# Kernel optimization log

Hardware: AMD Instinct MI355X
Metric: run time of the kernel (lower is better)

Reference implementation:

```python
import jax, jax.numpy as jnp
import numpy as np

B, N, C, H = 8, 4096, 768, 32
D = C // H  # head_dim = 24
EPS = 1e-12


def _l2norm(t):
    # F.normalize(dim=-1): t / max(||t||_2, eps)
    n = jnp.sqrt(jnp.sum(t * t, axis=-1, keepdims=True))
    return t / jnp.maximum(n, EPS)


def setup_inputs() -> dict:
    key = jax.random.key(0)
    ks = jax.random.split(key, 6)
    s_in = 1.0 / np.sqrt(C)
    return {
        "x": jax.random.normal(ks[0], (B, N, C), dtype=jnp.float32),
        "W_qkv": jax.random.uniform(ks[1], (C, 3 * C), jnp.float32, -s_in, s_in),
        "b_qkv": jax.random.uniform(ks[2], (3 * C,), jnp.float32, -s_in, s_in),
        "temperature": jnp.ones((H, 1, 1), dtype=jnp.float32),
        "W_proj": jax.random.uniform(ks[3], (C, C), jnp.float32, -s_in, s_in),
        "b_proj": jax.random.uniform(ks[4], (C,), jnp.float32, -s_in, s_in),
    }


def reference(x, W_qkv, b_qkv, temperature, W_proj, b_proj):
    b, n, c = x.shape
    qkv = x @ W_qkv + b_qkv                                  # (B,N,3C)
    qkv = qkv.reshape(b, n, 3, H, D).transpose(2, 0, 3, 1, 4)  # (3,B,H,N,D)
    q, k, v = qkv[0], qkv[1], qkv[2]                         # (B,H,N,D)
    q = jnp.swapaxes(q, -1, -2)                              # (B,H,D,N)
    k = jnp.swapaxes(k, -1, -2)
    v = jnp.swapaxes(v, -1, -2)
    q = _l2norm(q)                                           # normalize over N
    k = _l2norm(k)
    attn = jnp.einsum('bhdn,bhen->bhde', q, k) * temperature  # (B,H,D,D)
    attn = jax.nn.softmax(attn, axis=-1)
    y = jnp.einsum('bhde,bhen->bhdn', attn, v)               # (B,H,D,N)
    # Faithful to torch: (1,B,H,D,N).transpose(1,2).reshape(B,N,C)
    # == (H,B,D,N) flattened row-major into (B,N,C)
    y = jnp.transpose(y, (1, 0, 2, 3)).reshape(b, n, c)
    return y @ W_proj + b_proj
```

## Files before the change

kernel.cpp:

```cpp
#include <hip/hip_runtime.h>
#include <hip/hip_bf16.h>


#define DEVI __device__ __forceinline__

typedef __attribute__((ext_vector_type(8))) short bf16x8;
typedef __attribute__((ext_vector_type(4))) float f32x4;
typedef unsigned int u32;
typedef unsigned short u16;

DEVI u16 f2bf(float f) {
  union { float f; u32 u; } x; x.f = f;
  u32 r = x.u + 0x7FFFu + ((x.u >> 16) & 1u);
  return (u16)(r >> 16);
}

DEVI void gload_lds16(const void* g, void* l) {
  __builtin_amdgcn_global_load_lds((__attribute__((address_space(1))) void*)g,
                                   (__attribute__((address_space(3))) void*)l, 16, 0, 0);
}

__global__ __launch_bounds__(256) void cvt_kernel(const float* __restrict__ in,
                                                  u16* __restrict__ out, int n8) {
  int i = blockIdx.x * 256 + threadIdx.x;
  if (i >= n8) return;
  long o = (long)i * 8;
  float4 a = *(const float4*)(in + o);
  float4 b = *(const float4*)(in + o + 4);
  uint4 v;
  v.x = f2bf(a.x) | ((u32)f2bf(a.y) << 16);
  v.y = f2bf(a.z) | ((u32)f2bf(a.w) << 16);
  v.z = f2bf(b.x) | ((u32)f2bf(b.y) << 16);
  v.w = f2bf(b.z) | ((u32)f2bf(b.w) << 16);
  *(uint4*)(out + o) = v;
}

__global__ __launch_bounds__(256) void transpose_cvt(const float* __restrict__ W,
                                                     u16* __restrict__ Wt, int K, int N) {
  __shared__ float tile[32][33];
  int n0 = blockIdx.x * 32, k0 = blockIdx.y * 32;
  int tx = threadIdx.x, ty = threadIdx.y;
  #pragma unroll
  for (int i = 0; i < 4; ++i)
    tile[ty + 8 * i][tx] = W[(long)(k0 + ty + 8 * i) * N + n0 + tx];
  __syncthreads();
  #pragma unroll
  for (int i = 0; i < 4; ++i)
    Wt[(long)(n0 + ty + 8 * i) * K + k0 + tx] = f2bf(tile[tx][ty + 8 * i]);
}

template<int NT, int BF16_OUT>
__global__ __launch_bounds__(512, 4) void gemm2b_kernel(
    const u16* __restrict__ A, const u16* __restrict__ Bt,
    const float* __restrict__ bias, void* __restrict__ Cout,
    int M, int N) {
  constexpr int K = NT * 32;
  __shared__ __attribute__((aligned(128))) char lds[49152];

  int nbx = N >> 8;
  int nwg = gridDim.x;
  int bid = blockIdx.x;
  bid = (bid & 7) * (nwg >> 3) + (bid >> 3);
  int bx = bid % nbx, by = bid / nbx;

  int t = threadIdx.x;
  int w = t >> 6, l = t & 63;
  int wr = w >> 2, wc = w & 3;
  int l16 = l & 15, l4 = l >> 4;

  int cbb = (l4 * 16) ^ ((l16 & 8) << 2);
  int pA0 = (wr * 64 + l16) * 64 + cbb;
  int pB0 = 16384 + (wc * 64 + l16) * 64 + cbb;

  int pa = t * 16;
  int la = pa ^ (((pa >> 9) & 1) << 5);
  int soffA = (la >> 6) * K + ((la & 63) >> 1);
  int soffB[2];
  #pragma unroll
  for (int j = 0; j < 2; ++j) {
    int p = (j * 512 + t) * 16;
    int lb = p ^ (((p >> 9) & 1) << 5);
    soffB[j] = (lb >> 6) * K + ((lb & 63) >> 1);
  }

  const u16* Ag = A + (long)by * 128 * K;
  const u16* Bg = Bt + (long)bx * 256 * K;
  int sdst = w * 1024;

  f32x4 acc[4][4] = {};

  gload_lds16(Ag + soffA, lds + sdst);
  #pragma unroll
  for (int j = 0; j < 2; ++j)
    gload_lds16(Bg + soffB[j], lds + 16384 + j * 8192 + sdst);

  for (int kt = 0; kt < NT; ++kt) {
    int s = kt & 1;
    if (kt + 1 < NT) {
      gload_lds16(Ag + soffA + (kt + 1) * 32, lds + (s ^ 1) * 8192 + sdst);
      #pragma unroll
      for (int j = 0; j < 2; ++j)
        gload_lds16(Bg + soffB[j] + (kt + 1) * 32,
                    lds + 16384 + (s ^ 1) * 16384 + j * 8192 + sdst);
      asm volatile("s_waitcnt vmcnt(3)" ::: "memory");
    } else {
      asm volatile("s_waitcnt vmcnt(0)" ::: "memory");
    }
    __builtin_amdgcn_sched_barrier(0);
    __builtin_amdgcn_s_barrier();
    __builtin_amdgcn_sched_barrier(0);

    bf16x8 aF[4], bF[4];
    #pragma unroll
    for (int mi = 0; mi < 4; ++mi)
      aF[mi] = *(const bf16x8*)(lds + s * 8192 + mi * 1024 + pA0);
    #pragma unroll
    for (int n = 0; n < 4; ++n)
      bF[n] = *(const bf16x8*)(lds + s * 16384 + n * 1024 + pB0);

    __builtin_amdgcn_s_setprio(1);
    #pragma unroll
    for (int mi = 0; mi < 4; ++mi)
      #pragma unroll
      for (int n = 0; n < 4; ++n)
        acc[mi][n] = __builtin_amdgcn_mfma_f32_16x16x32_bf16(aF[mi], bF[n], acc[mi][n], 0, 0, 0);
    __builtin_amdgcn_s_setprio(0);
    __builtin_amdgcn_s_barrier();
    __builtin_amdgcn_sched_barrier(0);
  }

  #pragma unroll
  for (int mi = 0; mi < 4; ++mi) {
    int row0 = by * 128 + wr * 64 + mi * 16 + l4 * 4;
    #pragma unroll
    for (int n = 0; n < 4; ++n) {
      int col = bx * 256 + wc * 64 + n * 16 + l16;
      float bv = bias[col];
      #pragma unroll
      for (int j = 0; j < 4; ++j) {
        long idx = (long)(row0 + j) * N + col;
        float v = acc[mi][n][j] + bv;
        if (BF16_OUT) __builtin_nontemporal_store(f2bf(v), (u16*)Cout + idx);
        else          __builtin_nontemporal_store(v, (float*)Cout + idx);
      }
    }
  }
}

#define PFQK(nc, rq, rk)                                                       \
  { long cb = (long)(nc) * 294912;                                             \
    _Pragma("unroll") for (int i = 0; i < 6; ++i) {                            \
      rq[i] = *(const u32*)(qbase + cb + offi[i]);                             \
      rk[i] = *(const u32*)(qbase + cb + offi[i] + 768); } }

#define WRQK(rq, rk)                                                           \
  { _Pragma("unroll") for (int i = 0; i < 6; ++i) {                            \
      qt[dv[i] * 2][nv[i]] = (u16)rq[i];                                       \
      qt[dv[i] * 2 + 1][nv[i]] = (u16)(rq[i] >> 16);                           \
      kt[dv[i] * 2][nv[i]] = (u16)rk[i];                                       \
      kt[dv[i] * 2 + 1][nv[i]] = (u16)(rk[i] >> 16); } }

#define GRAM_MFMA                                                              \
  { _Pragma("unroll") for (int ks = 0; ks < 4; ++ks) {                         \
      int koff = ks * 32 + l4 * 8;                                             \
      bf16x8 qa = *(const bf16x8*)&qt[fm * 16 + l16][koff];                    \
      bf16x8 qb = *(const bf16x8*)&qt[fn * 16 + l16][koff];                    \
      bf16x8 ka = *(const bf16x8*)&kt[fm * 16 + l16][koff];                    \
      bf16x8 kb = *(const bf16x8*)&kt[fn * 16 + l16][koff];                    \
      accG = __builtin_amdgcn_mfma_f32_16x16x32_bf16(qa, kb, accG, 0, 0, 0);   \
      accQ = __builtin_amdgcn_mfma_f32_16x16x32_bf16(qa, qb, accQ, 0, 0, 0);   \
      accK = __builtin_amdgcn_mfma_f32_16x16x32_bf16(ka, kb, accK, 0, 0, 0); } }

#define PFV(nc, rv)                                                            \
  { long cb = (long)(nc) * 294912;                                             \
    _Pragma("unroll") for (int i = 0; i < 6; ++i)                              \
      rv[i] = *(const u32*)(vbase + cb + offi[i]); }

#define WRV(rv)                                                                \
  { _Pragma("unroll") for (int i = 0; i < 6; ++i)                              \
      *(u32*)&vl[nv[i]][dv[i] * 2] = rv[i]; }

#define PV_STORE(nc)                                                           \
  { int n0 = (nc) * 128;                                                       \
    f32x4 z = {};                                                              \
    _Pragma("unroll") for (int fnn = 0; fnn < 2; ++fnn) {                      \
      int ncol = w * 32 + fnn * 16 + l16;                                      \
      bf16x8 bv = *(const bf16x8*)&vl[ncol][l4 * 8];                           \
      f32x4 y0 = __builtin_amdgcn_mfma_f32_16x16x32_bf16(af0, bv, z, 0, 0, 0); \
      f32x4 y1 = __builtin_amdgcn_mfma_f32_16x16x32_bf16(af1, bv, z, 0, 0, 0); \
      int gn = n0 + ncol;                                                      \
      _Pragma("unroll") for (int j = 0; j < 4; ++j) {                          \
        int d0 = l4 * 4 + j;                                                   \
        ybase[(long)d0 * 4096 + gn] = f2bf(y0[j]);                             \
        int d1 = 16 + d0;                                                      \
        if (d1 < 24) ybase[(long)d1 * 4096 + gn] = f2bf(y1[j]); } } }

__global__ __launch_bounds__(256) void attn_kernel(const u16* __restrict__ qkv,
                                                   const float* __restrict__ temperature,
                                                   u16* __restrict__ yout) {
  __shared__ u16 qt[32][136];
  __shared__ u16 kt[32][136];
  __shared__ u16 vl[128][40];
  __shared__ u16 attnb[32][40];
  __shared__ float Gs[32][33];
  __shared__ float sq[32];
  __shared__ float sk[32];

  int bid = blockIdx.x;
  int b = bid >> 5, h = bid & 31;
  int t = threadIdx.x;
  int w = t >> 6, l = t & 63;
  int l16 = l & 15, l4 = l >> 4;
  int fm = w >> 1, fn = w & 1;

  for (int i = t; i < 32 * 136; i += 256) { qt[0][i] = 0; kt[0][i] = 0; }
  for (int i = t; i < 128 * 40; i += 256) vl[0][i] = 0;
  for (int i = t; i < 32 * 40; i += 256) attnb[0][i] = 0;

  int nv[6], dv[6], offi[6];
  #pragma unroll
  for (int i = 0; i < 6; ++i) {
    int idx = t + 256 * i;
    nv[i] = idx / 12; dv[i] = idx % 12;
    offi[i] = nv[i] * 2304 + dv[i] * 2;
  }

  f32x4 accG = {}, accQ = {}, accK = {};
  const u16* qbase = qkv + (long)b * 4096 * 2304 + h * 24;
  const u16* vbase = qbase + 1536;

  u32 rqA[6], rkA[6], rqB[6], rkB[6];
  PFQK(0, rqA, rkA);
  PFQK(1, rqB, rkB);
  __syncthreads();

  for (int nc = 0; nc < 32; nc += 2) {
    WRQK(rqA, rkA);
    __syncthreads();
    if (nc + 2 < 32) PFQK(nc + 2, rqA, rkA);
    GRAM_MFMA;
    __syncthreads();
    WRQK(rqB, rkB);
    __syncthreads();
    if (nc + 3 < 32) PFQK(nc + 3, rqB, rkB);
    GRAM_MFMA;
    __syncthreads();
  }

  #pragma unroll
  for (int j = 0; j < 4; ++j) Gs[fm * 16 + l4 * 4 + j][fn * 16 + l16] = accG[j];
  if (fm == fn) {
    #pragma unroll
    for (int j = 0; j < 4; ++j)
      if (l4 * 4 + j == l16) { sq[fm * 16 + l16] = accQ[j]; sk[fm * 16 + l16] = accK[j]; }
  }
  __syncthreads();

  if (t < 24) {
    float nq = fmaxf(sqrtf(fmaxf(sq[t], 0.f)), 1e-12f);
    float tmp = temperature[h];
    float p[24]; float mx = -1e30f;
    #pragma unroll
    for (int e = 0; e < 24; ++e) {
      float nk = fmaxf(sqrtf(fmaxf(sk[e], 0.f)), 1e-12f);
      float a = Gs[t][e] / (nq * nk) * tmp;
      p[e] = a; mx = fmaxf(mx, a);
    }
    float s = 0.f;
    #pragma unroll
    for (int e = 0; e < 24; ++e) { p[e] = __expf(p[e] - mx); s += p[e]; }
    float inv = 1.f / s;
    #pragma unroll
    for (int e = 0; e < 24; ++e) attnb[t][e] = f2bf(p[e] * inv);
  }

  u32 rvA[6], rvB[6];
  PFV(0, rvA);
  PFV(1, rvB);
  __syncthreads();

  bf16x8 af0 = *(const bf16x8*)&attnb[l16][l4 * 8];
  bf16x8 af1 = *(const bf16x8*)&attnb[16 + l16][l4 * 8];
  u16* ybase = yout + (long)(h * 8 + b) * 24 * 4096;

  for (int nc = 0; nc < 32; nc += 2) {
    WRV(rvA);
    __syncthreads();
    if (nc + 2 < 32) PFV(nc + 2, rvA);
    PV_STORE(nc);
    __syncthreads();
    WRV(rvB);
    __syncthreads();
    if (nc + 3 < 32) PFV(nc + 3, rvB);
    PV_STORE(nc + 1);
    __syncthreads();
  }
}

extern "C" void kernel_launch(void* const* d_in, const int* in_sizes, int n_in,
                              void* d_out, int out_size, void* d_ws, size_t ws_size,
                              hipStream_t stream) {
  const float* x     = (const float*)d_in[0];
  const float* Wqkv  = (const float*)d_in[1];
  const float* bqkv  = (const float*)d_in[2];
  const float* temp  = (const float*)d_in[3];
  const float* Wproj = (const float*)d_in[4];
  const float* bproj = (const float*)d_in[5];
  float* out = (float*)d_out;

  char* ws = (char*)d_ws;
  u16* xb  = (u16*)(ws);
  u16* wqt = (u16*)(ws + 50331648);
  u16* wpt = (u16*)(ws + 53870592);
  u16* qkv = (u16*)(ws + 55050240);
  u16* y   = xb;

  cvt_kernel<<<12288, 256, 0, stream>>>(x, xb, 3145728);
  transpose_cvt<<<dim3(72, 24), dim3(32, 8), 0, stream>>>(Wqkv, wqt, 768, 2304);
  transpose_cvt<<<dim3(24, 24), dim3(32, 8), 0, stream>>>(Wproj, wpt, 768, 768);
  gemm2b_kernel<24, 1><<<2304, 512, 0, stream>>>(xb, wqt, bqkv, qkv, 32768, 2304);
  attn_kernel<<<256, 256, 0, stream>>>(qkv, temp, y);
  gemm2b_kernel<24, 0><<<768, 512, 0, stream>>>(y, wpt, bproj, out, 32768, 768);
}
```

Baseline: 320.1 us.

## Triple-buffer GEMM K pipeline, widen attention chunk loads to 16-byte vectors

The bf16 GEMM moves from double to triple buffering in LDS, with two K tiles in flight and the loop fully unrolled, to hide more global load latency. The cost is more LDS per block (72KB), which may reduce occupancy. The attention kernel now processes 256-token chunks with uint4 (16-byte) loads instead of 4-byte loads, halving loop iterations and barriers, at the price of larger LDS tiles. The bf16 GEMM output store also changes from nontemporal to a regular store, so the qkv result can stay in cache for the attention kernel that reads it next.

```diff
diff --git a/kernel.cpp b/kernel.cpp
--- a/kernel.cpp
+++ b/kernel.cpp
@@ -49,13 +49,19 @@
     Wt[(long)(n0 + ty + 8 * i) * K + k0 + tx] = f2bf(tile[tx][ty + 8 * i]);
 }
 
+#define STAGE_T(ktile, slot)                                                   \
+  { gload_lds16(Ag + soffA + (ktile) * 32, lds + (slot) * 8192 + sdst);        \
+    _Pragma("unroll") for (int j_ = 0; j_ < 2; ++j_)                           \
+      gload_lds16(Bg + soffB[j_] + (ktile) * 32,                               \
+                  lds + 24576 + (slot) * 16384 + j_ * 8192 + sdst); }
+
 template<int NT, int BF16_OUT>
 __global__ __launch_bounds__(512, 4) void gemm2b_kernel(
     const u16* __restrict__ A, const u16* __restrict__ Bt,
     const float* __restrict__ bias, void* __restrict__ Cout,
     int M, int N) {
   constexpr int K = NT * 32;
-  __shared__ __attribute__((aligned(128))) char lds[49152];
+  __shared__ __attribute__((aligned(128))) char lds[73728];
 
   int nbx = N >> 8;
   int nwg = gridDim.x;
@@ -70,7 +76,7 @@
 
   int cbb = (l4 * 16) ^ ((l16 & 8) << 2);
   int pA0 = (wr * 64 + l16) * 64 + cbb;
-  int pB0 = 16384 + (wc * 64 + l16) * 64 + cbb;
+  int pB0 = (wc * 64 + l16) * 64 + cbb;
 
   int pa = t * 16;
   int la = pa ^ (((pa >> 9) & 1) << 5);
@@ -89,19 +95,16 @@
 
   f32x4 acc[4][4] = {};
 
-  gload_lds16(Ag + soffA, lds + sdst);
-  #pragma unroll
-  for (int j = 0; j < 2; ++j)
-    gload_lds16(Bg + soffB[j], lds + 16384 + j * 8192 + sdst);
-
+  STAGE_T(0, 0);
+  STAGE_T(1, 1);
+
+  #pragma unroll
   for (int kt = 0; kt < NT; ++kt) {
-    int s = kt & 1;
-    if (kt + 1 < NT) {
-      gload_lds16(Ag + soffA + (kt + 1) * 32, lds + (s ^ 1) * 8192 + sdst);
-      #pragma unroll
-      for (int j = 0; j < 2; ++j)
-        gload_lds16(Bg + soffB[j] + (kt + 1) * 32,
-                    lds + 16384 + (s ^ 1) * 16384 + j * 8192 + sdst);
+    int rs = kt % 3;
+    if (kt + 2 < NT) {
+      STAGE_T(kt + 2, (kt + 2) % 3);
+      asm volatile("s_waitcnt vmcnt(6)" ::: "memory");
+    } else if (kt + 2 == NT) {
       asm volatile("s_waitcnt vmcnt(3)" ::: "memory");
     } else {
       asm volatile("s_waitcnt vmcnt(0)" ::: "memory");
@@ -113,10 +116,10 @@
     bf16x8 aF[4], bF[4];
     #pragma unroll
     for (int mi = 0; mi < 4; ++mi)
-      aF[mi] = *(const bf16x8*)(lds + s * 8192 + mi * 1024 + pA0);
+      aF[mi] = *(const bf16x8*)(lds + rs * 8192 + mi * 1024 + pA0);
     #pragma unroll
     for (int n = 0; n < 4; ++n)
-      bF[n] = *(const bf16x8*)(lds + s * 16384 + n * 1024 + pB0);
+      bF[n] = *(const bf16x8*)(lds + 24576 + rs * 16384 + n * 1024 + pB0);
 
     __builtin_amdgcn_s_setprio(1);
     #pragma unroll
@@ -140,7 +143,7 @@
       for (int j = 0; j < 4; ++j) {
         long idx = (long)(row0 + j) * N + col;
         float v = acc[mi][n][j] + bv;
-        if (BF16_OUT) __builtin_nontemporal_store(f2bf(v), (u16*)Cout + idx);
+        if (BF16_OUT) ((u16*)Cout)[idx] = f2bf(v);
         else          __builtin_nontemporal_store(v, (float*)Cout + idx);
       }
     }
@@ -148,20 +151,22 @@
 }
 
 #define PFQK(nc, rq, rk)                                                       \
-  { long cb = (long)(nc) * 294912;                                             \
-    _Pragma("unroll") for (int i = 0; i < 6; ++i) {                            \
-      rq[i] = *(const u32*)(qbase + cb + offi[i]);                             \
-      rk[i] = *(const u32*)(qbase + cb + offi[i] + 768); } }
+  { long cb = (long)(nc) * 589824;                                             \
+    _Pragma("unroll") for (int i = 0; i < 3; ++i) {                            \
+      rq[i] = *(const uint4*)(qbase + cb + offI[i]);                           \
+      rk[i] = *(const uint4*)(kbase + cb + offI[i]); } }
 
 #define WRQK(rq, rk)                                                           \
-  { _Pragma("unroll") for (int i = 0; i < 6; ++i) {                            \
-      qt[dv[i] * 2][nv[i]] = (u16)rq[i];                                       \
-      qt[dv[i] * 2 + 1][nv[i]] = (u16)(rq[i] >> 16);                           \
-      kt[dv[i] * 2][nv[i]] = (u16)rk[i];                                       \
-      kt[dv[i] * 2 + 1][nv[i]] = (u16)(rk[i] >> 16); } }
-
-#define GRAM_MFMA                                                              \
-  { _Pragma("unroll") for (int ks = 0; ks < 4; ++ks) {                         \
+  { _Pragma("unroll") for (int i = 0; i < 3; ++i) {                            \
+      const u32* pq = (const u32*)&rq[i];                                      \
+      const u32* pk = (const u32*)&rk[i];                                      \
+      _Pragma("unroll") for (int j = 0; j < 4; ++j) {                          \
+        int d = sI[i] * 8 + 2 * j;                                             \
+        qt[d][nI[i]] = (u16)pq[j]; qt[d + 1][nI[i]] = (u16)(pq[j] >> 16);      \
+        kt[d][nI[i]] = (u16)pk[j]; kt[d + 1][nI[i]] = (u16)(pk[j] >> 16); } } }
+
+#define GRAM8                                                                  \
+  { _Pragma("unroll") for (int ks = 0; ks < 8; ++ks) {                         \
       int koff = ks * 32 + l4 * 8;                                             \
       bf16x8 qa = *(const bf16x8*)&qt[fm * 16 + l16][koff];                    \
       bf16x8 qb = *(const bf16x8*)&qt[fn * 16 + l16][koff];                    \
@@ -172,19 +177,19 @@
       accK = __builtin_amdgcn_mfma_f32_16x16x32_bf16(ka, kb, accK, 0, 0, 0); } }
 
 #define PFV(nc, rv)                                                            \
-  { long cb = (long)(nc) * 294912;                                             \
-    _Pragma("unroll") for (int i = 0; i < 6; ++i)                              \
-      rv[i] = *(const u32*)(vbase + cb + offi[i]); }
+  { long cb = (long)(nc) * 589824;                                             \
+    _Pragma("unroll") for (int i = 0; i < 3; ++i)                              \
+      rv[i] = *(const uint4*)(vbase + cb + offI[i]); }
 
 #define WRV(rv)                                                                \
-  { _Pragma("unroll") for (int i = 0; i < 6; ++i)                              \
-      *(u32*)&vl[nv[i]][dv[i] * 2] = rv[i]; }
+  { _Pragma("unroll") for (int i = 0; i < 3; ++i)                              \
+      *(uint4*)&vl[nI[i]][sI[i] * 8] = rv[i]; }
 
 #define PV_STORE(nc)                                                           \
-  { int n0 = (nc) * 128;                                                       \
+  { int n0 = (nc) * 256;                                                       \
     f32x4 z = {};                                                              \
-    _Pragma("unroll") for (int fnn = 0; fnn < 2; ++fnn) {                      \
-      int ncol = w * 32 + fnn * 16 + l16;                                      \
+    _Pragma("unroll") for (int fnn = 0; fnn < 4; ++fnn) {                      \
+      int ncol = w * 64 + fnn * 16 + l16;                                      \
       bf16x8 bv = *(const bf16x8*)&vl[ncol][l4 * 8];                           \
       f32x4 y0 = __builtin_amdgcn_mfma_f32_16x16x32_bf16(af0, bv, z, 0, 0, 0); \
       f32x4 y1 = __builtin_amdgcn_mfma_f32_16x16x32_bf16(af1, bv, z, 0, 0, 0); \
@@ -198,9 +203,9 @@
 __global__ __launch_bounds__(256) void attn_kernel(const u16* __restrict__ qkv,
                                                    const float* __restrict__ temperature,
                                                    u16* __restrict__ yout) {
-  __shared__ u16 qt[32][136];
-  __shared__ u16 kt[32][136];
-  __shared__ u16 vl[128][40];
+  __shared__ u16 qt[32][272];
+  __shared__ u16 kt[32][272];
+  __shared__ u16 vl[256][40];
   __shared__ u16 attnb[32][40];
   __shared__ float Gs[32][33];
   __shared__ float sq[32];
@@ -213,37 +218,38 @@
   int l16 = l & 15, l4 = l >> 4;
   int fm = w >> 1, fn = w & 1;
 
-  for (int i = t; i < 32 * 136; i += 256) { qt[0][i] = 0; kt[0][i] = 0; }
-  for (int i = t; i < 128 * 40; i += 256) vl[0][i] = 0;
+  for (int i = t; i < 32 * 272; i += 256) { qt[0][i] = 0; kt[0][i] = 0; }
+  for (int i = t; i < 256 * 40; i += 256) vl[0][i] = 0;
   for (int i = t; i < 32 * 40; i += 256) attnb[0][i] = 0;
 
-  int nv[6], dv[6], offi[6];
-  #pragma unroll
-  for (int i = 0; i < 6; ++i) {
+  int nI[3], sI[3], offI[3];
+  #pragma unroll
+  for (int i = 0; i < 3; ++i) {
     int idx = t + 256 * i;
-    nv[i] = idx / 12; dv[i] = idx % 12;
-    offi[i] = nv[i] * 2304 + dv[i] * 2;
+    nI[i] = idx / 3; sI[i] = idx % 3;
+    offI[i] = nI[i] * 2304 + sI[i] * 8;
   }
 
   f32x4 accG = {}, accQ = {}, accK = {};
   const u16* qbase = qkv + (long)b * 4096 * 2304 + h * 24;
+  const u16* kbase = qbase + 768;
   const u16* vbase = qbase + 1536;
 
-  u32 rqA[6], rkA[6], rqB[6], rkB[6];
+  uint4 rqA[3], rkA[3], rqB[3], rkB[3];
   PFQK(0, rqA, rkA);
   PFQK(1, rqB, rkB);
   __syncthreads();
 
-  for (int nc = 0; nc < 32; nc += 2) {
+  for (int nc = 0; nc < 16; nc += 2) {
     WRQK(rqA, rkA);
     __syncthreads();
-    if (nc + 2 < 32) PFQK(nc + 2, rqA, rkA);
-    GRAM_MFMA;
+    if (nc + 2 < 16) PFQK(nc + 2, rqA, rkA);
+    GRAM8;
     __syncthreads();
     WRQK(rqB, rkB);
     __syncthreads();
-    if (nc + 3 < 32) PFQK(nc + 3, rqB, rkB);
-    GRAM_MFMA;
+    if (nc + 3 < 16) PFQK(nc + 3, rqB, rkB);
+    GRAM8;
     __syncthreads();
   }
 
@@ -274,7 +280,7 @@
     for (int e = 0; e < 24; ++e) attnb[t][e] = f2bf(p[e] * inv);
   }
 
-  u32 rvA[6], rvB[6];
+  uint4 rvA[3], rvB[3];
   PFV(0, rvA);
   PFV(1, rvB);
   __syncthreads();
@@ -283,15 +289,15 @@
   bf16x8 af1 = *(const bf16x8*)&attnb[16 + l16][l4 * 8];
   u16* ybase = yout + (long)(h * 8 + b) * 24 * 4096;
 
-  for (int nc = 0; nc < 32; nc += 2) {
+  for (int nc = 0; nc < 16; nc += 2) {
     WRV(rvA);
     __syncthreads();
-    if (nc + 2 < 32) PFV(nc + 2, rvA);
+    if (nc + 2 < 16) PFV(nc + 2, rvA);
     PV_STORE(nc);
     __syncthreads();
     WRV(rvB);
     __syncthreads();
-    if (nc + 3 < 32) PFV(nc + 3, rvB);
+    if (nc + 3 < 16) PFV(nc + 3, rvB);
     PV_STORE(nc + 1);
     __syncthreads();
   }
```

Measured after the change: 309.6 us. 3.3% less time.
